# Optimization experiments

Hardware: AMD Instinct MI355X
Metric: run time of the kernel (lower is better)

The kernel has to match this reference:

```python
import jax, jax.numpy as jnp
import numpy as np

NUM_SITES = 64
BOND_DIM = 64
PHYS_DIM = 2
BATCH = 8192
INIT_STD = 0.125  # 1/sqrt(bond_dim)
EPS_AMP = 1e-12
EPS_LOG = 1e-30


def setup_inputs() -> dict:
    key = jax.random.key(0)
    k_cfg, k_l, k_b, k_r = jax.random.split(key, 4)
    configurations = jax.random.randint(k_cfg, (BATCH, NUM_SITES), 0, PHYS_DIM, dtype=jnp.int32)
    left = jax.random.normal(k_l, (PHYS_DIM, BOND_DIM), dtype=jnp.float32) * INIT_STD
    bulk = jax.random.normal(k_b, (NUM_SITES - 2, BOND_DIM, PHYS_DIM, BOND_DIM), dtype=jnp.float32) * INIT_STD
    right = jax.random.normal(k_r, (BOND_DIM, PHYS_DIM), dtype=jnp.float32) * INIT_STD
    return {"configurations": configurations, "left": left, "bulk": bulk, "right": right}


def _psi(configurations, left, bulk, right):
    # configurations: [B, S] int; left: [d, D]; bulk: [S-2, D, d, D]; right: [D, d]
    B = configurations.shape[0]
    env0 = left[configurations[:, 0]]  # [B, D]
    cfg_mid = configurations[:, 1:-1].T  # [S-2, B]

    def step(env, xs):
        site_t, idx = xs  # site_t: [D, d, D], idx: [B]
        D = site_t.shape[0]
        # env @ site (contract left bond), then gather the per-sample physical slice
        tmp = (env @ site_t.reshape(D, -1)).reshape(B, PHYS_DIM, D)  # [B, d, D]
        env = jnp.take_along_axis(tmp, idx[:, None, None], axis=1)[:, 0, :]  # [B, D]
        return env, None

    env, _ = jax.lax.scan(step, env0, (bulk, cfg_mid))
    cols = jnp.take(right, configurations[:, -1], axis=1).T  # [B, D]
    return jnp.sum(env * cols, axis=1)  # [B]


def _log_norm(left, bulk, right):
    env0 = left.T @ left  # [D, D]  (real dtype -> conj trivial)

    def step(carry, site_t):
        env, log_scale = carry
        sm = jnp.transpose(site_t, (1, 0, 2))  # [d, D, D]
        env = jnp.einsum('pdi,de,pej->ij', sm, env, sm)  # sum_p A_p^H env A_p
        scale = jnp.maximum(jnp.max(jnp.abs(env)), EPS_LOG)
        return (env / scale, log_scale + jnp.log(scale)), None

    (env, log_scale), _ = jax.lax.scan(step, (env0, jnp.zeros((), left.dtype)), bulk)
    z = jnp.sum(right * (env @ right))
    return jnp.log(jnp.maximum(z, EPS_LOG)) + log_scale


def reference(configurations, left, bulk, right):
    psi = _psi(configurations, left, bulk, right)
    abs_sq = jnp.maximum(psi * psi, EPS_AMP)
    log_z = _log_norm(left, bulk, right)
    nll = -(jnp.log(abs_sq) - log_z)
    return jnp.mean(nll)
```

## Files before the change

kernel.cpp:

```cpp
#include <hip/hip_runtime.h>
#include <math.h>

#define NBULK 62
#define SB    72

typedef __attribute__((ext_vector_type(8))) short bf8_t;
typedef __attribute__((ext_vector_type(4))) float f4_t;

#define MFMA(a, b, c) __builtin_amdgcn_mfma_f32_16x16x32_bf16((a), (b), (c), 0, 0, 0)

__device__ __forceinline__ unsigned short f2bf(float f) {
    unsigned int u = __float_as_uint(f);
    return (unsigned short)((u + 0x7FFFu + ((u >> 16) & 1u)) >> 16);
}
__device__ __forceinline__ float bf2f(unsigned short h) {
    return __uint_as_float(((unsigned int)h) << 16);
}

__device__ __forceinline__ void gload16(const void* g, void* l) {
    __builtin_amdgcn_global_load_lds(
        (const __attribute__((address_space(1))) unsigned int*)g,
        (__attribute__((address_space(3))) unsigned int*)l, 16, 0, 0);
}

#define WS_E_OFF   1024
#define WS_B_OFF   6144
#define WS_BT_OFF  45056
#define WS_MR_OFF  1060864


extern "C" __global__ __launch_bounds__(256)
void mps_precompute(const float* __restrict__ bulkG,
                    unsigned short* __restrict__ BTg,
                    unsigned short* __restrict__ MRg)
{
    __shared__ unsigned short BTl[8192];
    __shared__ unsigned short MRl[8192];
    const int s = blockIdx.x, tid = threadIdx.x;
    const float4* src = (const float4*)(bulkG + (size_t)s * 8192);
    for (int c = 0; c < 8; ++c) {
        int idx = tid + c * 256;
        float4 v = src[idx];
        int f  = idx * 4;
        int kk = f >> 7;
        int p  = (f >> 6) & 1;
        int j  = f & 63;
        unsigned short b0 = f2bf(v.x), b1 = f2bf(v.y), b2 = f2bf(v.z), b3 = f2bf(v.w);
        int n = p * 64 + kk;
        int off = n * 64 + (((j >> 3) ^ (n & 7)) << 3) + (j & 7);
        MRl[off + 0] = b0; MRl[off + 1] = b1; MRl[off + 2] = b2; MRl[off + 3] = b3;
        unsigned short bb[4] = {b0, b1, b2, b3};
        #pragma unroll
        for (int t2 = 0; t2 < 4; ++t2) {
            int n2 = p * 64 + j + t2;
            BTl[n2 * 64 + (((kk >> 3) ^ (n2 & 7)) << 3) + (kk & 7)] = bb[t2];
        }
    }
    __syncthreads();
    const uint4* bt4 = (const uint4*)BTl;
    const uint4* mr4 = (const uint4*)MRl;
    uint4* btg = (uint4*)(BTg + (size_t)s * 8192);
    uint4* mrg = (uint4*)(MRg + (size_t)s * 8192);
    for (int c = 0; c < 4; ++c) {
        int idx = tid + c * 256;
        btg[idx] = bt4[idx];
        mrg[idx] = mr4[idx];
    }
}

extern "C" __global__ __launch_bounds__(256)
void mps_main(const int* __restrict__ cfgG, const float* __restrict__ leftG,
              const float* __restrict__ rightG, float* __restrict__ wsF,
              const unsigned short* __restrict__ BTg,
              const unsigned short* __restrict__ MRg)
{
    extern __shared__ char smem[];
    unsigned short* smem16 = (unsigned short*)smem;
    const int tid  = threadIdx.x;
    const int bid  = blockIdx.x;
    const int wv   = tid >> 6;
    const int lane = tid & 63;
    const int quad = lane >> 4;
    const int ln   = lane & 15;

    if (bid >= 2) {
        unsigned short* Bb0  = smem16;
        unsigned short* Bb1  = Bb0 + 8192;
        unsigned short* env  = Bb1 + 8192;
        unsigned char*  selT = (unsigned char*)(env + 64 * SB);

        const int s0 = (bid - 2) * 64;
        {
            int m = tid >> 2, part = tid & 3;
            const int* row = cfgG + (size_t)(s0 + m) * 64 + part * 16;
            #pragma unroll
            for (int q = 0; q < 4; ++q) {
                int4 v = *(const int4*)(row + q * 4);
                int cb = part * 16 + q * 4;
                selT[(cb + 0) * 64 + m] = (unsigned char)v.x;
                selT[(cb + 1) * 64 + m] = (unsigned char)v.y;
                selT[(cb + 2) * 64 + m] = (unsigned char)v.z;
                selT[(cb + 3) * 64 + m] = (unsigned char)v.w;
            }
        }
        {
            const char* g0 = (const char*)BTg;
            for (int c = 0; c < 4; ++c) {
                int chunk = wv * 4 + c;
                gload16(g0 + chunk * 1024 + (size_t)lane * 16, (char*)Bb0 + chunk * 1024);
            }
        }
        __syncthreads();

        bf8_t Af[2];
        {
            int sel0 = selT[0 * 64 + wv * 16 + ln];
            const float* lp0 = leftG + sel0 * 64;
            #pragma unroll
            for (int h = 0; h < 2; ++h) {
                float4 a = *(const float4*)(lp0 + h * 32 + quad * 8);
                float4 b = *(const float4*)(lp0 + h * 32 + quad * 8 + 4);
                bf8_t t;
                t[0] = (short)f2bf(a.x); t[1] = (short)f2bf(a.y);
                t[2] = (short)f2bf(a.z); t[3] = (short)f2bf(a.w);
                t[4] = (short)f2bf(b.x); t[5] = (short)f2bf(b.y);
                t[6] = (short)f2bf(b.z); t[7] = (short)f2bf(b.w);
                Af[h] = t;
            }
        }

        for (int t = 0; t < NBULK; ++t) {
            __syncthreads();
            unsigned short* B = (t & 1) ? Bb1 : Bb0;
            if (t + 1 < NBULK) {
                const char* gn = (const char*)(BTg + (size_t)(t + 1) * 8192);
                char* l = (char*)((t & 1) ? Bb0 : Bb1);
                for (int c = 0; c < 4; ++c) {
                    int chunk = wv * 4 + c;
                    gload16(gn + chunk * 1024 + (size_t)lane * 16, l + chunk * 1024);
                }
            }
            bf8_t Bf[2][4][2];
            #pragma unroll
            for (int b2 = 0; b2 < 2; ++b2)
                #pragma unroll
                for (int ct = 0; ct < 4; ++ct) {
                    int row = b2 * 64 + ct * 16 + ln;
                    #pragma unroll
                    for (int h = 0; h < 2; ++h)
                        Bf[b2][ct][h] = *(const bf8_t*)(B + row * 64 + (((h * 4 + quad) ^ (ln & 7)) << 3));
                }
            f4_t acc[2][4];
            #pragma unroll
            for (int b2 = 0; b2 < 2; ++b2)
                #pragma unroll
                for (int ct = 0; ct < 4; ++ct) {
                    f4_t a = {0.f, 0.f, 0.f, 0.f};
                    a = MFMA(Af[0], Bf[b2][ct][0], a);
                    a = MFMA(Af[1], Bf[b2][ct][1], a);
                    acc[b2][ct] = a;
                }
            unsigned int sv = *(const unsigned int*)(selT + (t + 1) * 64 + wv * 16 + quad * 4);
            #pragma unroll
            for (int ct = 0; ct < 4; ++ct)
                #pragma unroll
                for (int r = 0; r < 4; ++r) {
                    float v = ((sv >> (8 * r)) & 1u) ? acc[1][ct][r] : acc[0][ct][r];
                    env[(wv * 16 + quad * 4 + r) * SB + ct * 16 + ln] = f2bf(v);
                }
            Af[0] = *(const bf8_t*)(env + (wv * 16 + ln) * SB + quad * 8);
            Af[1] = *(const bf8_t*)(env + (wv * 16 + ln) * SB + 32 + quad * 8);
        }
        {
            int selL = selT[63 * 64 + wv * 16 + ln];
            bf8_t e0 = *(const bf8_t*)(env + (wv * 16 + ln) * SB + quad * 16);
            bf8_t e1 = *(const bf8_t*)(env + (wv * 16 + ln) * SB + quad * 16 + 8);
            float p = 0.f;
            #pragma unroll
            for (int j = 0; j < 8; ++j)
                p = fmaf(bf2f((unsigned short)e0[j]), rightG[(quad * 16 + j) * 2 + selL], p);
            #pragma unroll
            for (int j = 0; j < 8; ++j)
                p = fmaf(bf2f((unsigned short)e1[j]), rightG[(quad * 16 + 8 + j) * 2 + selL], p);
            p += __shfl_xor(p, 16);
            p += __shfl_xor(p, 32);
            float lp = logf(fmaxf(p * p, 1e-12f));
            lp += __shfl_xor(lp, 1); lp += __shfl_xor(lp, 2);
            lp += __shfl_xor(lp, 4); lp += __shfl_xor(lp, 8);
            if (lane == 0) atomicAdd(&wsF[0], lp);
        }
    } else {
        unsigned short* Ebf = smem16;
        unsigned short* St0 = Ebf + 64 * SB;
        unsigned short* St1 = St0 + 64 * SB;
        unsigned short* Ms0 = St1 + 64 * SB;
        unsigned short* Ms1 = Ms0 + 8192;
        float* wred = (float*)(Ms1 + 8192);

        const bool fwd = (bid == 0);
        const unsigned short* srcbase = fwd ? BTg : MRg;
        {
            int i = tid >> 2, jq = tid & 3;
            for (int jj = 0; jj < 16; ++jj) {
                int j = jq * 16 + jj;
                float v;
                if (fwd) v = leftG[i] * leftG[j] + leftG[64 + i] * leftG[64 + j];
                else     v = rightG[i * 2] * rightG[j * 2] + rightG[i * 2 + 1] * rightG[j * 2 + 1];
                Ebf[i * SB + j] = f2bf(v);
            }
        }
        {
            int st = fwd ? 0 : 61;
            const char* g = (const char*)(srcbase + (size_t)st * 8192);
            for (int c = 0; c < 4; ++c) {
                int chunk = wv * 4 + c;
                gload16(g + chunk * 1024 + (size_t)lane * 16, (char*)Ms0 + chunk * 1024);
            }
        }
        float lsum = 0.f;
        const int p   = wv >> 1;
        const int ntb = (wv & 1) * 2;
        const int mta = (wv >> 1) * 2;
        const int nta = (wv & 1) * 2;
        unsigned short* Stp = p ? St1 : St0;

        for (int k = 0; k < 31; ++k) {
            __syncthreads();
            unsigned short* M = (k & 1) ? Ms1 : Ms0;
            if (k + 1 < 31) {
                int sn = fwd ? (k + 1) : (61 - (k + 1));
                const char* g = (const char*)(srcbase + (size_t)sn * 8192);
                char* l = (char*)((k & 1) ? Ms0 : Ms1);
                for (int c = 0; c < 4; ++c) {
                    int chunk = wv * 4 + c;
                    gload16(g + chunk * 1024 + (size_t)lane * 16, l + chunk * 1024);
                }
            }
            float inv = 1.f;
            if (k > 0) {
                const float* wp = wred + ((k - 1) & 1) * 4;
                float mm = fmaxf(fmaxf(wp[0], wp[1]), fmaxf(wp[2], wp[3]));
                float sc = fmaxf(mm, 1e-30f);
                inv = 1.f / sc;
                if (tid == 0) lsum += logf(sc);
            }
            {
                bf8_t Af2[4][2];
                #pragma unroll
                for (int mt = 0; mt < 4; ++mt)
                    #pragma unroll
                    for (int h = 0; h < 2; ++h)
                        Af2[mt][h] = *(const bf8_t*)(Ebf + (mt * 16 + ln) * SB + h * 32 + quad * 8);
                #pragma unroll
                for (int c = 0; c < 2; ++c) {
                    int nt = ntb + c;
                    int row = p * 64 + nt * 16 + ln;
                    bf8_t B0 = *(const bf8_t*)(M + row * 64 + (((0 + quad) ^ (ln & 7)) << 3));
                    bf8_t B1 = *(const bf8_t*)(M + row * 64 + (((4 + quad) ^ (ln & 7)) << 3));
                    #pragma unroll
                    for (int mt = 0; mt < 4; ++mt) {
                        f4_t a = {0.f, 0.f, 0.f, 0.f};
                        a = MFMA(Af2[mt][0], B0, a);
                        a = MFMA(Af2[mt][1], B1, a);
                        ushort4 pk;
                        pk.x = f2bf(a[0]); pk.y = f2bf(a[1]); pk.z = f2bf(a[2]); pk.w = f2bf(a[3]);
                        *(ushort4*)(Stp + (nt * 16 + ln) * SB + mt * 16 + quad * 4) = pk;
                    }
                }
            }
            __syncthreads();
            {
                bf8_t Aw[2][2][2], Bw[2][2][2];
                #pragma unroll
                for (int pp = 0; pp < 2; ++pp)
                    #pragma unroll
                    for (int mi = 0; mi < 2; ++mi)
                        #pragma unroll
                        for (int h = 0; h < 2; ++h)
                            Aw[pp][mi][h] = *(const bf8_t*)(M + (pp * 64 + (mta + mi) * 16 + ln) * 64
                                                              + (((h * 4 + quad) ^ (ln & 7)) << 3));
                #pragma unroll
                for (int pp = 0; pp < 2; ++pp)
                    #pragma unroll
                    for (int ni = 0; ni < 2; ++ni)
                        #pragma unroll
                        for (int h = 0; h < 2; ++h)
                            Bw[pp][ni][h] = *(const bf8_t*)((pp ? St1 : St0)
                                                            + ((nta + ni) * 16 + ln) * SB + h * 32 + quad * 8);
                float mx = 0.f;
                #pragma unroll
                for (int mi = 0; mi < 2; ++mi)
                    #pragma unroll
                    for (int ni = 0; ni < 2; ++ni) {
                        f4_t a = {0.f, 0.f, 0.f, 0.f};
                        #pragma unroll
                        for (int pp = 0; pp < 2; ++pp)
                            #pragma unroll
                            for (int h = 0; h < 2; ++h)
                                a = MFMA(Aw[pp][mi][h], Bw[pp][ni][h], a);
                        #pragma unroll
                        for (int r = 0; r < 4; ++r) {
                            float val = a[r] * inv;
                            mx = fmaxf(mx, fabsf(val));
                            Ebf[((mta + mi) * 16 + quad * 4 + r) * SB + (nta + ni) * 16 + ln] = f2bf(val);
                        }
                    }
                #pragma unroll
                for (int off = 32; off > 0; off >>= 1)
                    mx = fmaxf(mx, __shfl_xor(mx, off));
                if (lane == 0) wred[(k & 1) * 4 + wv] = mx;
            }
        }
        __syncthreads();
        float* dst = wsF + (fwd ? WS_E_OFF : WS_B_OFF);
        for (int c = 0; c < 16; ++c) {
            int idx = tid + c * 256;
            dst[idx] = bf2f(Ebf[(idx >> 6) * SB + (idx & 63)]);
        }
        if (tid == 0) wsF[fwd ? 1 : 2] = lsum;
    }
}

extern "C" __global__ void mps_finalize(const float* __restrict__ wsF, float* __restrict__ out)
{
    const int lane = threadIdx.x;
    const float* E  = wsF + WS_E_OFF;
    const float* Bm = wsF + WS_B_OFF;
    float a = 0.f;
    #pragma unroll 8
    for (int j = 0; j < 64; ++j)
        a = fmaf(E[lane * 64 + j], Bm[lane * 64 + j], a);
    #pragma unroll
    for (int off = 32; off > 0; off >>= 1)
        a += __shfl_down(a, off);
    if (lane == 0) {
        const float z = fmaxf(a, 1e-30f);
        const float log_z = logf(z) + wsF[1] + wsF[2];
        out[0] = log_z - wsF[0] * (1.0f / 8192.0f);
    }
}

extern "C" void kernel_launch(void* const* d_in, const int* in_sizes, int n_in,
                              void* d_out, int out_size, void* d_ws, size_t ws_size,
                              hipStream_t stream)
{
    const int*   cfg   = (const int*)d_in[0];
    const float* left  = (const float*)d_in[1];
    const float* bulk  = (const float*)d_in[2];
    const float* right = (const float*)d_in[3];
    float* wsF = (float*)d_ws;
    unsigned short* BTg = (unsigned short*)((char*)d_ws + WS_BT_OFF);
    unsigned short* MRg = (unsigned short*)((char*)d_ws + WS_MR_OFF);

    hipMemsetAsync(d_ws, 0, 16, stream);
    mps_precompute<<<dim3(62), dim3(256), 0, stream>>>(bulk, BTg, MRg);
    mps_main<<<dim3(130), dim3(256), 60480, stream>>>(cfg, left, right, wsF, BTg, MRg);
    mps_finalize<<<dim3(1), dim3(64), 0, stream>>>(wsF, (float*)d_out);
}
```

Before: 119.2 us.

## Restructure psi chain to per-wave 32x32 MFMA with register-resident site tensors

The psi contraction is rewritten so each of two waves handles 32 samples using 32x32x16 bf16 MFMAs. Site tensors are loaded straight from global memory into registers with a two-deep prefetch, which removes the LDS double buffer and the per-step block-wide barriers. Config bits are packed into 32-bit masks, and bf16 packing uses v_cvt_pk_bf16_f32. It also drops the hipMemset by zeroing the accumulators inside the precompute kernel, transposes the norm-chain store layout, and replaces one __syncthreads with a raw barrier; two of every four waves in the psi blocks now sit idle, which lowers occupancy.

```diff
diff --git a/kernel.cpp b/kernel.cpp
--- a/kernel.cpp
+++ b/kernel.cpp
@@ -6,8 +6,10 @@
 
 typedef __attribute__((ext_vector_type(8))) short bf8_t;
 typedef __attribute__((ext_vector_type(4))) float f4_t;
-
-#define MFMA(a, b, c) __builtin_amdgcn_mfma_f32_16x16x32_bf16((a), (b), (c), 0, 0, 0)
+typedef __attribute__((ext_vector_type(16))) float f16v_t;
+
+#define MFMA16(a, b, c) __builtin_amdgcn_mfma_f32_16x16x32_bf16((a), (b), (c), 0, 0, 0)
+#define MFMA32(a, b, c) __builtin_amdgcn_mfma_f32_32x32x16_bf16((a), (b), (c), 0, 0, 0)
 
 __device__ __forceinline__ unsigned short f2bf(float f) {
     unsigned int u = __float_as_uint(f);
@@ -15,6 +17,11 @@
 }
 __device__ __forceinline__ float bf2f(unsigned short h) {
     return __uint_as_float(((unsigned int)h) << 16);
+}
+__device__ __forceinline__ unsigned cvtpk(float lo, float hi) {
+    unsigned r;
+    asm("v_cvt_pk_bf16_f32 %0, %1, %2" : "=v"(r) : "v"(lo), "v"(hi));
+    return r;
 }
 
 __device__ __forceinline__ void gload16(const void* g, void* l) {
@@ -32,11 +39,15 @@
 extern "C" __global__ __launch_bounds__(256)
 void mps_precompute(const float* __restrict__ bulkG,
                     unsigned short* __restrict__ BTg,
-                    unsigned short* __restrict__ MRg)
+                    unsigned short* __restrict__ MRg,
+                    float* __restrict__ wsF)
 {
     __shared__ unsigned short BTl[8192];
     __shared__ unsigned short MRl[8192];
     const int s = blockIdx.x, tid = threadIdx.x;
+    if (s == 0 && tid == 0) {
+        wsF[0] = 0.f; wsF[1] = 0.f; wsF[2] = 0.f; wsF[3] = 0.f;
+    }
     const float4* src = (const float4*)(bulkG + (size_t)s * 8192);
     for (int c = 0; c < 8; ++c) {
         int idx = tid + c * 256;
@@ -68,6 +79,50 @@
     }
 }
 
+__device__ __forceinline__ void psi_phase(
+    uint4 (&R)[16], int tt, unsigned short* env, const char* BTb,
+    const int (&off)[4], unsigned selLo, unsigned selHi,
+    int s, int hi, int e7, const f16v_t& Z)
+{
+    bf8_t benv[4];
+    #pragma unroll
+    for (int ks = 0; ks < 4; ++ks)
+        benv[ks] = *(const bf8_t*)((const char*)env + s * 128 + (((ks * 2 + hi) ^ e7) << 4));
+    unsigned sbit = (tt + 1 < 32) ? (selLo >> (tt + 1)) : (selHi >> (tt - 31));
+    const bool takeB = (sbit & 1u) != 0u;
+    #pragma unroll
+    for (int jt = 0; jt < 2; ++jt) {
+        f16v_t a0 = Z, a1 = Z;
+        #pragma unroll
+        for (int ks = 0; ks < 4; ++ks) {
+            a0 = MFMA32(*(const bf8_t*)&R[jt * 4 + ks],     benv[ks], a0);
+            a1 = MFMA32(*(const bf8_t*)&R[8 + jt * 4 + ks], benv[ks], a1);
+        }
+        #pragma unroll
+        for (int b = 0; b < 4; ++b) {
+            float v0 = takeB ? a1[4 * b + 0] : a0[4 * b + 0];
+            float v1 = takeB ? a1[4 * b + 1] : a0[4 * b + 1];
+            float v2 = takeB ? a1[4 * b + 2] : a0[4 * b + 2];
+            float v3 = takeB ? a1[4 * b + 3] : a0[4 * b + 3];
+            uint2 w;
+            w.x = cvtpk(v0, v1);
+            w.y = cvtpk(v2, v3);
+            *(uint2*)((char*)env + s * 128 + (((jt * 4 + b) ^ e7) << 4) + hi * 8) = w;
+        }
+    }
+    if (tt + 2 < NBULK) {
+        const char* tb = BTb + (size_t)(tt + 2) * 16384;
+        #pragma unroll
+        for (int p = 0; p < 2; ++p)
+            #pragma unroll
+            for (int jt = 0; jt < 2; ++jt)
+                #pragma unroll
+                for (int ks = 0; ks < 4; ++ks)
+                    R[p * 8 + jt * 4 + ks] =
+                        *(const uint4*)(tb + p * 8192 + jt * 4096 + off[ks]);
+    }
+}
+
 extern "C" __global__ __launch_bounds__(256)
 void mps_main(const int* __restrict__ cfgG, const float* __restrict__ leftG,
               const float* __restrict__ rightG, float* __restrict__ wsF,
@@ -80,113 +135,86 @@
     const int bid  = blockIdx.x;
     const int wv   = tid >> 6;
     const int lane = tid & 63;
-    const int quad = lane >> 4;
-    const int ln   = lane & 15;
 
     if (bid >= 2) {
-        unsigned short* Bb0  = smem16;
-        unsigned short* Bb1  = Bb0 + 8192;
-        unsigned short* env  = Bb1 + 8192;
-        unsigned char*  selT = (unsigned char*)(env + 64 * SB);
-
-        const int s0 = (bid - 2) * 64;
-        {
-            int m = tid >> 2, part = tid & 3;
-            const int* row = cfgG + (size_t)(s0 + m) * 64 + part * 16;
-            #pragma unroll
-            for (int q = 0; q < 4; ++q) {
-                int4 v = *(const int4*)(row + q * 4);
-                int cb = part * 16 + q * 4;
-                selT[(cb + 0) * 64 + m] = (unsigned char)v.x;
-                selT[(cb + 1) * 64 + m] = (unsigned char)v.y;
-                selT[(cb + 2) * 64 + m] = (unsigned char)v.z;
-                selT[(cb + 3) * 64 + m] = (unsigned char)v.w;
-            }
-        }
-        {
-            const char* g0 = (const char*)BTg;
-            for (int c = 0; c < 4; ++c) {
-                int chunk = wv * 4 + c;
-                gload16(g0 + chunk * 1024 + (size_t)lane * 16, (char*)Bb0 + chunk * 1024);
-            }
-        }
-        __syncthreads();
-
-        bf8_t Af[2];
-        {
-            int sel0 = selT[0 * 64 + wv * 16 + ln];
-            const float* lp0 = leftG + sel0 * 64;
-            #pragma unroll
-            for (int h = 0; h < 2; ++h) {
-                float4 a = *(const float4*)(lp0 + h * 32 + quad * 8);
-                float4 b = *(const float4*)(lp0 + h * 32 + quad * 8 + 4);
-                bf8_t t;
-                t[0] = (short)f2bf(a.x); t[1] = (short)f2bf(a.y);
-                t[2] = (short)f2bf(a.z); t[3] = (short)f2bf(a.w);
-                t[4] = (short)f2bf(b.x); t[5] = (short)f2bf(b.y);
-                t[6] = (short)f2bf(b.z); t[7] = (short)f2bf(b.w);
-                Af[h] = t;
-            }
-        }
-
-        for (int t = 0; t < NBULK; ++t) {
-            __syncthreads();
-            unsigned short* B = (t & 1) ? Bb1 : Bb0;
-            if (t + 1 < NBULK) {
-                const char* gn = (const char*)(BTg + (size_t)(t + 1) * 8192);
-                char* l = (char*)((t & 1) ? Bb0 : Bb1);
-                for (int c = 0; c < 4; ++c) {
-                    int chunk = wv * 4 + c;
-                    gload16(gn + chunk * 1024 + (size_t)lane * 16, l + chunk * 1024);
+        if (wv >= 2) return;
+        const int s  = lane & 31;
+        const int hi = lane >> 5;
+        const int e7 = lane & 7;
+        unsigned short* env = smem16 + wv * 2048;
+        const int s0 = (bid - 2) * 64 + wv * 32;
+
+        int off[4];
+        #pragma unroll
+        for (int ks = 0; ks < 4; ++ks)
+            off[ks] = s * 128 + (((ks * 2 + hi) ^ e7) << 4);
+
+        const char* BTb = (const char*)BTg;
+        uint4 ra[16], rb[16];
+        #pragma unroll
+        for (int p = 0; p < 2; ++p)
+            #pragma unroll
+            for (int jt = 0; jt < 2; ++jt)
+                #pragma unroll
+                for (int ks = 0; ks < 4; ++ks) {
+                    ra[p * 8 + jt * 4 + ks] = *(const uint4*)(BTb + p * 8192 + jt * 4096 + off[ks]);
+                    rb[p * 8 + jt * 4 + ks] = *(const uint4*)(BTb + 16384 + p * 8192 + jt * 4096 + off[ks]);
                 }
-            }
-            bf8_t Bf[2][4][2];
-            #pragma unroll
-            for (int b2 = 0; b2 < 2; ++b2)
-                #pragma unroll
-                for (int ct = 0; ct < 4; ++ct) {
-                    int row = b2 * 64 + ct * 16 + ln;
-                    #pragma unroll
-                    for (int h = 0; h < 2; ++h)
-                        Bf[b2][ct][h] = *(const bf8_t*)(B + row * 64 + (((h * 4 + quad) ^ (ln & 7)) << 3));
-                }
-            f4_t acc[2][4];
-            #pragma unroll
-            for (int b2 = 0; b2 < 2; ++b2)
-                #pragma unroll
-                for (int ct = 0; ct < 4; ++ct) {
-                    f4_t a = {0.f, 0.f, 0.f, 0.f};
-                    a = MFMA(Af[0], Bf[b2][ct][0], a);
-                    a = MFMA(Af[1], Bf[b2][ct][1], a);
-                    acc[b2][ct] = a;
-                }
-            unsigned int sv = *(const unsigned int*)(selT + (t + 1) * 64 + wv * 16 + quad * 4);
-            #pragma unroll
-            for (int ct = 0; ct < 4; ++ct)
-                #pragma unroll
-                for (int r = 0; r < 4; ++r) {
-                    float v = ((sv >> (8 * r)) & 1u) ? acc[1][ct][r] : acc[0][ct][r];
-                    env[(wv * 16 + quad * 4 + r) * SB + ct * 16 + ln] = f2bf(v);
-                }
-            Af[0] = *(const bf8_t*)(env + (wv * 16 + ln) * SB + quad * 8);
-            Af[1] = *(const bf8_t*)(env + (wv * 16 + ln) * SB + 32 + quad * 8);
-        }
-        {
-            int selL = selT[63 * 64 + wv * 16 + ln];
-            bf8_t e0 = *(const bf8_t*)(env + (wv * 16 + ln) * SB + quad * 16);
-            bf8_t e1 = *(const bf8_t*)(env + (wv * 16 + ln) * SB + quad * 16 + 8);
-            float p = 0.f;
-            #pragma unroll
-            for (int j = 0; j < 8; ++j)
-                p = fmaf(bf2f((unsigned short)e0[j]), rightG[(quad * 16 + j) * 2 + selL], p);
-            #pragma unroll
-            for (int j = 0; j < 8; ++j)
-                p = fmaf(bf2f((unsigned short)e1[j]), rightG[(quad * 16 + 8 + j) * 2 + selL], p);
-            p += __shfl_xor(p, 16);
-            p += __shfl_xor(p, 32);
-            float lp = logf(fmaxf(p * p, 1e-12f));
-            lp += __shfl_xor(lp, 1); lp += __shfl_xor(lp, 2);
-            lp += __shfl_xor(lp, 4); lp += __shfl_xor(lp, 8);
+
+        unsigned mbits = 0;
+        {
+            const int4* crow = (const int4*)(cfgG + (size_t)(s0 + s) * 64 + hi * 32);
+            #pragma unroll
+            for (int c = 0; c < 8; ++c) {
+                int4 v = crow[c];
+                mbits |= (unsigned)(v.x & 1) << (c * 4 + 0);
+                mbits |= (unsigned)(v.y & 1) << (c * 4 + 1);
+                mbits |= (unsigned)(v.z & 1) << (c * 4 + 2);
+                mbits |= (unsigned)(v.w & 1) << (c * 4 + 3);
+            }
+        }
+        unsigned other = __shfl_xor(mbits, 32);
+        unsigned selLo = hi ? other : mbits;
+        unsigned selHi = hi ? mbits : other;
+
+        {
+            const float* lp = leftG + (selLo & 1u) * 64 + hi * 32;
+            #pragma unroll
+            for (int gg = 0; gg < 4; ++gg) {
+                float4 a = *(const float4*)(lp + gg * 8);
+                float4 b = *(const float4*)(lp + gg * 8 + 4);
+                uint4 w;
+                w.x = (unsigned)f2bf(a.x) | ((unsigned)f2bf(a.y) << 16);
+                w.y = (unsigned)f2bf(a.z) | ((unsigned)f2bf(a.w) << 16);
+                w.z = (unsigned)f2bf(b.x) | ((unsigned)f2bf(b.y) << 16);
+                w.w = (unsigned)f2bf(b.z) | ((unsigned)f2bf(b.w) << 16);
+                int g = hi * 4 + gg;
+                *(uint4*)((char*)env + s * 128 + ((g ^ e7) << 4)) = w;
+            }
+        }
+
+        const f16v_t Z = {0.f};
+        for (int t = 0; t < NBULK; t += 2) {
+            psi_phase(ra, t,     env, BTb, off, selLo, selHi, s, hi, e7, Z);
+            psi_phase(rb, t + 1, env, BTb, off, selLo, selHi, s, hi, e7, Z);
+        }
+
+        {
+            int selL = (selHi >> 31) & 1;
+            float psum = 0.f;
+            #pragma unroll
+            for (int gg = 0; gg < 4; ++gg) {
+                int g = hi * 4 + gg;
+                bf8_t e = *(const bf8_t*)((const char*)env + s * 128 + ((g ^ e7) << 4));
+                #pragma unroll
+                for (int j = 0; j < 8; ++j)
+                    psum = fmaf(bf2f((unsigned short)e[j]), rightG[(g * 8 + j) * 2 + selL], psum);
+            }
+            psum += __shfl_xor(psum, 32);
+            float lp = logf(fmaxf(psum * psum, 1e-12f));
+            if (hi) lp = 0.f;
+            #pragma unroll
+            for (int o = 1; o < 64; o <<= 1) lp += __shfl_xor(lp, o);
             if (lane == 0) atomicAdd(&wsF[0], lp);
         }
     } else {
@@ -197,6 +225,8 @@
         unsigned short* Ms1 = Ms0 + 8192;
         float* wred = (float*)(Ms1 + 8192);
 
+        const int quad = lane >> 4;
+        const int ln   = lane & 15;
         const bool fwd = (bid == 0);
         const unsigned short* srcbase = fwd ? BTg : MRg;
         {
@@ -260,15 +290,17 @@
                     #pragma unroll
                     for (int mt = 0; mt < 4; ++mt) {
                         f4_t a = {0.f, 0.f, 0.f, 0.f};
-                        a = MFMA(Af2[mt][0], B0, a);
-                        a = MFMA(Af2[mt][1], B1, a);
+                        a = MFMA16(Af2[mt][0], B0, a);
+                        a = MFMA16(Af2[mt][1], B1, a);
                         ushort4 pk;
                         pk.x = f2bf(a[0]); pk.y = f2bf(a[1]); pk.z = f2bf(a[2]); pk.w = f2bf(a[3]);
                         *(ushort4*)(Stp + (nt * 16 + ln) * SB + mt * 16 + quad * 4) = pk;
                     }
                 }
             }
-            __syncthreads();
+            asm volatile("s_waitcnt lgkmcnt(0)" ::: "memory");
+            __builtin_amdgcn_s_barrier();
+            __builtin_amdgcn_sched_barrier(0);
             {
                 bf8_t Aw[2][2][2], Bw[2][2][2];
                 #pragma unroll
@@ -297,17 +329,16 @@
                         for (int pp = 0; pp < 2; ++pp)
                             #pragma unroll
                             for (int h = 0; h < 2; ++h)
-                                a = MFMA(Aw[pp][mi][h], Bw[pp][ni][h], a);
-                        #pragma unroll
-                        for (int r = 0; r < 4; ++r) {
-                            float val = a[r] * inv;
-                            mx = fmaxf(mx, fabsf(val));
-                            Ebf[((mta + mi) * 16 + quad * 4 + r) * SB + (nta + ni) * 16 + ln] = f2bf(val);
-                        }
+                                a = MFMA16(Aw[pp][mi][h], Bw[pp][ni][h], a);
+                        float x0 = a[0] * inv, x1 = a[1] * inv, x2 = a[2] * inv, x3 = a[3] * inv;
+                        mx = fmaxf(mx, fmaxf(fmaxf(fabsf(x0), fabsf(x1)), fmaxf(fabsf(x2), fabsf(x3))));
+                        ushort4 pk;
+                        pk.x = f2bf(x0); pk.y = f2bf(x1); pk.z = f2bf(x2); pk.w = f2bf(x3);
+                        *(ushort4*)(Ebf + ((nta + ni) * 16 + ln) * SB + (mta + mi) * 16 + quad * 4) = pk;
                     }
                 #pragma unroll
-                for (int off = 32; off > 0; off >>= 1)
-                    mx = fmaxf(mx, __shfl_xor(mx, off));
+                for (int off2 = 32; off2 > 0; off2 >>= 1)
+                    mx = fmaxf(mx, __shfl_xor(mx, off2));
                 if (lane == 0) wred[(k & 1) * 4 + wv] = mx;
             }
         }
@@ -352,8 +383,7 @@
     unsigned short* BTg = (unsigned short*)((char*)d_ws + WS_BT_OFF);
     unsigned short* MRg = (unsigned short*)((char*)d_ws + WS_MR_OFF);
 
-    hipMemsetAsync(d_ws, 0, 16, stream);
-    mps_precompute<<<dim3(62), dim3(256), 0, stream>>>(bulk, BTg, MRg);
+    mps_precompute<<<dim3(62), dim3(256), 0, stream>>>(bulk, BTg, MRg, wsF);
     mps_main<<<dim3(130), dim3(256), 60480, stream>>>(cfg, left, right, wsF, BTg, MRg);
     mps_finalize<<<dim3(1), dim3(64), 0, stream>>>(wsF, (float*)d_out);
 }
```

New measurement: 119.0 us. No clear change (-0.2%).
